# Optimization experiments

Hardware: AMD Instinct MI355X
Metric: run time of the kernel (lower is better)

Reference implementation:

```python
import jax, jax.numpy as jnp
import numpy as np

D = 1024
H = 16
HD = D // H
SCALE = HD ** -0.5
EPS = 1e-5


def _layernorm(x, g, b):
    mu = jnp.mean(x, axis=-1, keepdims=True)
    var = jnp.var(x, axis=-1, keepdims=True)
    return (x - mu) * jax.lax.rsqrt(var + EPS) * g + b


def setup_inputs() -> dict:
    key = jax.random.key(0)
    ks = jax.random.split(key, 10)
    B, L = 2, 2048
    x = jax.random.normal(ks[0], (B, L, D), dtype=jnp.float32)
    s = 1.0 / np.sqrt(D)
    w_qkv = jax.random.normal(ks[1], (D, 3 * D), dtype=jnp.float32) * s
    w_out = jax.random.normal(ks[2], (D, D), dtype=jnp.float32) * s
    w1 = jax.random.normal(ks[3], (D, 2 * D), dtype=jnp.float32) * s
    b1 = jnp.zeros((2 * D,), dtype=jnp.float32)
    w2 = jax.random.normal(ks[4], (2 * D, D), dtype=jnp.float32) / np.sqrt(2 * D)
    b2 = jnp.zeros((D,), dtype=jnp.float32)
    g1 = jnp.ones((D,), dtype=jnp.float32)
    be1 = jnp.zeros((D,), dtype=jnp.float32)
    g2 = jnp.ones((D,), dtype=jnp.float32)
    be2 = jnp.zeros((D,), dtype=jnp.float32)
    return {"x": x, "w_qkv": w_qkv, "w_out": w_out, "w1": w1, "b1": b1,
            "w2": w2, "b2": b2, "g1": g1, "be1": be1, "g2": g2, "be2": be2}


def reference(x, w_qkv, w_out, w1, b1, w2, b2, g1, be1, g2, be2):
    B, L, _ = x.shape
    qkv = (x @ w_qkv).reshape(B, L, 3, H, HD)
    q, k, v = jnp.moveaxis(qkv, 2, 0)          # each [B, L, H, HD]
    # scores: [B, H, L, L]
    attn = jnp.einsum('bqhd,bkhd->bhqk', q, k) * SCALE
    causal = jnp.tril(jnp.ones((L, L), dtype=bool))
    attn = jnp.where(causal[None, None], attn, -jnp.inf)
    attn = jax.nn.softmax(attn, axis=-1)
    out = jnp.einsum('bhqk,bkhd->bqhd', attn, v).reshape(B, L, D)
    out = out @ w_out
    x = _layernorm(x + out, g1, be1)
    ffn = jax.nn.gelu(x @ w1 + b1, approximate=False) @ w2 + b2
    x = _layernorm(x + ffn, g2, be2)
    return x
```

## Files before the change

kernel.cpp:

```cpp
#include <hip/hip_runtime.h>
#include <hip/hip_bf16.h>
#include <math.h>

#define L_SEQ 2048
#define NB 2
#define DM 1024
#define NHEAD 16
#define HDIM 64
#define QKV_LD 3072
#define RL 0.18033688011112042f
#define DTHR 44.3614f

typedef __attribute__((ext_vector_type(8))) __bf16 bf16x8;
typedef __attribute__((ext_vector_type(4))) __bf16 bf16x4;
typedef __attribute__((ext_vector_type(4))) float f32x4;
typedef __attribute__((ext_vector_type(16))) float f32x16;
typedef __attribute__((ext_vector_type(4))) unsigned int u32x4;

typedef __attribute__((address_space(3))) unsigned int lds_u32;
typedef const __attribute__((address_space(1))) unsigned int glob_u32;
#define GLD16(g, l) __builtin_amdgcn_global_load_lds((glob_u32*)(g), (lds_u32*)(l), 16, 0, 0)

__device__ __forceinline__ unsigned pack2(float a, float b) {
  unsigned short ua = __builtin_bit_cast(unsigned short, (__bf16)a);
  unsigned short ub = __builtin_bit_cast(unsigned short, (__bf16)b);
  return (unsigned)ua | ((unsigned)ub << 16);
}

__global__ __launch_bounds__(256) void prep_k(const float* __restrict__ w_qkv,
                                              const float* __restrict__ w_out,
                                              const float* __restrict__ w1,
                                              const float* __restrict__ w2,
                                              const float* __restrict__ x,
                                              __hip_bfloat16* __restrict__ wqT,
                                              __hip_bfloat16* __restrict__ woT,
                                              __hip_bfloat16* __restrict__ w1T,
                                              __hip_bfloat16* __restrict__ w2T,
                                              __hip_bfloat16* __restrict__ xb) {
  const int id = blockIdx.x;
  if (id >= 8192) {
    const size_t base = ((size_t)(id - 8192) * 256 + threadIdx.x) * 8;
    float4 a = *reinterpret_cast<const float4*>(x + base);
    float4 b = *reinterpret_cast<const float4*>(x + base + 4);
    bf16x8 o;
    o[0] = (__bf16)a.x; o[1] = (__bf16)a.y; o[2] = (__bf16)a.z; o[3] = (__bf16)a.w;
    o[4] = (__bf16)b.x; o[5] = (__bf16)b.y; o[6] = (__bf16)b.z; o[7] = (__bf16)b.w;
    *reinterpret_cast<bf16x8*>(xb + base) = o;
    return;
  }
  const float* W; __hip_bfloat16* WT; int K, N, kb, nb;
  if (id < 3072)      { W = w_qkv; WT = wqT; K = 1024; N = 3072; kb = id & 31;          nb = id >> 5; }
  else if (id < 4096) { W = w_out; WT = woT; K = 1024; N = 1024; kb = (id - 3072) & 31; nb = (id - 3072) >> 5; }
  else if (id < 6144) { W = w1;    WT = w1T; K = 1024; N = 2048; kb = (id - 4096) & 31; nb = (id - 4096) >> 5; }
  else                { W = w2;    WT = w2T; K = 2048; N = 1024; kb = (id - 6144) & 63; nb = (id - 6144) >> 6; }
  __shared__ float tsm[32][33];
  const int k0 = kb * 32, n0 = nb * 32;
  const int c = threadIdx.x & 31, r = threadIdx.x >> 5;
#pragma unroll
  for (int i = 0; i < 4; ++i)
    tsm[r + 8 * i][c] = W[(size_t)(k0 + r + 8 * i) * N + n0 + c];
  __syncthreads();
#pragma unroll
  for (int i = 0; i < 4; ++i)
    WT[(size_t)(n0 + r + 8 * i) * K + k0 + c] = __float2bfloat16(tsm[c][r + 8 * i]);
}

template<int EPI, int OUTB, int HASRES, int BN>
__global__ __launch_bounds__(256) void gemm2(const __hip_bfloat16* __restrict__ A,
                                             const __hip_bfloat16* __restrict__ BT,
                                             const float* __restrict__ bias,
                                             float* __restrict__ Cf,
                                             __hip_bfloat16* __restrict__ Cb,
                                             const float* __restrict__ RES,
                                             int M, int N, int K) {
  constexpr int MI = (BN == 128) ? 4 : 2;
  __shared__ __align__(16) __hip_bfloat16 As[128 * 32];
  __shared__ __align__(16) __hip_bfloat16 Bs[BN * 32];
  const int tid  = threadIdx.x;
  const int lane = tid & 63, wave = tid >> 6;
  const int wr = (BN == 128) ? (wave >> 1) : wave;
  const int wc = (BN == 128) ? (wave & 1) : 0;
  const int lr = lane & 15, lq = lane >> 4;
  const int bm0 = blockIdx.y * 128, bn0 = blockIdx.x * BN;
  f32x4 acc[MI][4] = {};

  for (int k0 = 0; k0 < K; k0 += 32) {
#pragma unroll
    for (int j = 0; j < 2; ++j) {
      const int cbase = j * 256 + wave * 64;
      const int c = cbase + lane;
      GLD16(A + (size_t)(bm0 + (c >> 2)) * K + k0 + (c & 3) * 8, (char*)As + cbase * 16);
    }
#pragma unroll
    for (int j = 0; j < BN / 64; ++j) {
      const int cbase = j * 256 + wave * 64;
      const int c = cbase + lane;
      GLD16(BT + (size_t)(bn0 + (c >> 2)) * K + k0 + (c & 3) * 8, (char*)Bs + cbase * 16);
    }
    __syncthreads();
    bf16x8 af[MI], bfr[4];
#pragma unroll
    for (int i = 0; i < MI; ++i)
      af[i] = *reinterpret_cast<const bf16x8*>(As + (wr * (MI * 16) + i * 16 + lr) * 32 + lq * 8);
#pragma unroll
    for (int i = 0; i < 4; ++i)
      bfr[i] = *reinterpret_cast<const bf16x8*>(Bs + (wc * 64 + i * 16 + lr) * 32 + lq * 8);
#pragma unroll
    for (int mi = 0; mi < MI; ++mi)
#pragma unroll
      for (int ni = 0; ni < 4; ++ni)
        acc[mi][ni] = __builtin_amdgcn_mfma_f32_16x16x32_bf16(af[mi], bfr[ni], acc[mi][ni], 0, 0, 0);
    __syncthreads();
  }

#pragma unroll
  for (int mi = 0; mi < MI; ++mi) {
#pragma unroll
    for (int ni = 0; ni < 4; ++ni) {
      const int col = bn0 + wc * 64 + ni * 16 + lr;
      const float bv = (EPI >= 1) ? bias[col] : 0.0f;
#pragma unroll
      for (int j = 0; j < 4; ++j) {
        const int row = bm0 + wr * (MI * 16) + mi * 16 + lq * 4 + j;
        float v = acc[mi][ni][j] + bv;
        if (HASRES) v += RES[(size_t)row * N + col];
        if (EPI == 2) v = 0.5f * v * (1.0f + erff(v * 0.70710678118654752f));
        if (OUTB) Cb[(size_t)row * N + col] = __float2bfloat16(v);
        else      Cf[(size_t)row * N + col] = v;
      }
    }
  }
}


#define DIAG_MASK(sv)                                                               \
  _Pragma("unroll")                                                                 \
  for (int r = 0; r < 16; ++r) {                                                    \
    const int kl = (r & 3) + 8 * (r >> 2) + 4 * hi;                                 \
    if (kl > lq32) sv[r] = -1e30f;                                                  \
  }

#define PV_HALF(wl0, wl1, wh0, wh1, ksg)                                            \
  {                                                                                 \
    unsigned t0_ = hi ? (wl0) : (wh0);                                              \
    unsigned t1_ = hi ? (wl1) : (wh1);                                              \
    t0_ = (unsigned)__shfl_xor((int)t0_, 32);                                       \
    t1_ = (unsigned)__shfl_xor((int)t1_, 32);                                       \
    u32x4 fw;                                                                       \
    fw[0] = hi ? t0_ : (wl0);  fw[1] = hi ? t1_ : (wl1);                            \
    fw[2] = hi ? (wh0) : t0_;  fw[3] = hi ? (wh1) : t1_;                            \
    bf16x8 pfb = __builtin_bit_cast(bf16x8, fw);                                    \
    const int krow_ = (ksg) * 16 + 8 * hi;                                          \
    bf16x8 vA, vB;                                                                  \
    _Pragma("unroll")                                                               \
    for (int j_ = 0; j_ < 8; ++j_) {                                                \
      vA[j_] = VwB[(krow_ + j_) * 64 + lq32];                                       \
      vB[j_] = VwB[(krow_ + j_) * 64 + 32 + lq32];                                  \
    }                                                                               \
    __builtin_amdgcn_s_setprio(1);                                                  \
    o0 = __builtin_amdgcn_mfma_f32_32x32x16_bf16(vA, pfb, o0, 0, 0, 0);             \
    o1 = __builtin_amdgcn_mfma_f32_32x32x16_bf16(vB, pfb, o1, 0, 0, 0);             \
    __builtin_amdgcn_s_setprio(0);                                                  \
  }

__global__ __launch_bounds__(256, 4) void attn_k(const __hip_bfloat16* __restrict__ qkv,
                                                 __hip_bfloat16* __restrict__ outb) {
  __shared__ __align__(16) char smem[4 * 8192 + 2048];
  const int bid = blockIdx.x;
  const int seq = bid >> 3;
  const int bh  = (bid & 7) * 4 + (seq & 3);
  const int qt32 = 63 - (seq >> 2);
  const int b = bh >> 4, h = bh & 15;
  const int qb = qt32 * 32;
  const int tid = threadIdx.x;
  const int lane = tid & 63, wave = tid >> 6;
  const int lq32 = lane & 31, hi = lane >> 5;
  const size_t rowbase = (size_t)(b * L_SEQ) * QKV_LD;
  char* const Vw = smem + wave * 8192;
  const __bf16* const VwB = (const __bf16*)Vw;
  float* const ML = (float*)(smem + 32768);

  bf16x8 qf[4];
  {
    const __hip_bfloat16* qp = qkv + rowbase + (size_t)(qb + lq32) * QKV_LD + h * HDIM + 8 * hi;
#pragma unroll
    for (int c = 0; c < 4; ++c) qf[c] = *reinterpret_cast<const bf16x8*>(qp + 16 * c);
  }

  f32x16 o0 = {}, o1 = {};
  float m = -1e30f, lsum = 0.0f;

  int t = wave;
  bf16x8 kr0, kr1, kr2, kr3;
  if (t <= qt32) {
    const __hip_bfloat16* kp = qkv + rowbase + (size_t)(t * 32 + lq32) * QKV_LD + DM + h * HDIM + 8 * hi;
    kr0 = *reinterpret_cast<const bf16x8*>(kp);
    kr1 = *reinterpret_cast<const bf16x8*>(kp + 16);
    kr2 = *reinterpret_cast<const bf16x8*>(kp + 32);
    kr3 = *reinterpret_cast<const bf16x8*>(kp + 48);
  }

  for (; t <= qt32; t += 4) {
    const int k0 = t * 32;
    const bool pf = (t + 4 <= qt32);
    bf16x8 kn0, kn1, kn2, kn3;
    if (pf) {
      const __hip_bfloat16* kp = qkv + rowbase + (size_t)(k0 + 128 + lq32) * QKV_LD + DM + h * HDIM + 8 * hi;
      kn0 = *reinterpret_cast<const bf16x8*>(kp);
      kn1 = *reinterpret_cast<const bf16x8*>(kp + 16);
      kn2 = *reinterpret_cast<const bf16x8*>(kp + 32);
      kn3 = *reinterpret_cast<const bf16x8*>(kp + 48);
    }
#pragma unroll
    for (int p = 0; p < 4; ++p)
      GLD16(qkv + rowbase + (size_t)(k0 + 8 * p + (lane >> 3)) * QKV_LD + 2 * DM + h * HDIM + (lane & 7) * 8,
            Vw + p * 1024);
    f32x16 s = {};
    __builtin_amdgcn_s_setprio(1);
    s = __builtin_amdgcn_mfma_f32_32x32x16_bf16(kr0, qf[0], s, 0, 0, 0);
    s = __builtin_amdgcn_mfma_f32_32x32x16_bf16(kr1, qf[1], s, 0, 0, 0);
    s = __builtin_amdgcn_mfma_f32_32x32x16_bf16(kr2, qf[2], s, 0, 0, 0);
    s = __builtin_amdgcn_mfma_f32_32x32x16_bf16(kr3, qf[3], s, 0, 0, 0);
    __builtin_amdgcn_s_setprio(0);
    if (t == qt32) { DIAG_MASK(s) }
    float a0 = fmaxf(s[0], s[1]),   a1 = fmaxf(s[2], s[3]);
    float a2 = fmaxf(s[4], s[5]),   a3 = fmaxf(s[6], s[7]);
    float a4 = fmaxf(s[8], s[9]),   a5 = fmaxf(s[10], s[11]);
    float a6 = fmaxf(s[12], s[13]), a7 = fmaxf(s[14], s[15]);
    a0 = fmaxf(a0, a1); a2 = fmaxf(a2, a3); a4 = fmaxf(a4, a5); a6 = fmaxf(a6, a7);
    float tm = fmaxf(fmaxf(a0, a2), fmaxf(a4, a6));
    tm = fmaxf(tm, __shfl_xor(tm, 32));
    if (!__all(tm <= m + DTHR)) {
      const float mn = fmaxf(m, tm);
      const float fac = __builtin_amdgcn_exp2f((m - mn) * RL);
      m = mn; lsum *= fac; o0 *= fac; o1 *= fac;
    }
    const float mneg = -m * RL;
    float rs = 0.0f;
#pragma unroll
    for (int r = 0; r < 16; ++r) {
      s[r] = __builtin_amdgcn_exp2f(fmaf(s[r], RL, mneg));
      rs += s[r];
    }
    rs += __shfl_xor(rs, 32);
    lsum += rs;
    unsigned w0 = pack2(s[0], s[1]),   w1 = pack2(s[2], s[3]);
    unsigned w2 = pack2(s[4], s[5]),   w3 = pack2(s[6], s[7]);
    unsigned w4 = pack2(s[8], s[9]),   w5 = pack2(s[10], s[11]);
    unsigned w6 = pack2(s[12], s[13]), w7 = pack2(s[14], s[15]);
    PV_HALF(w0, w1, w2, w3, 0)
    PV_HALF(w4, w5, w6, w7, 1)
    if (pf) { kr0 = kn0; kr1 = kn1; kr2 = kn2; kr3 = kn3; }
  }

  {
    float* Ow = (float*)Vw;
#pragma unroll
    for (int r = 0; r < 16; ++r) {
      const int d0 = (r & 3) + 8 * (r >> 2) + 4 * hi;
      Ow[d0 * 32 + lq32] = o0[r];
      Ow[(d0 + 32) * 32 + lq32] = o1[r];
    }
    if (hi == 0) {
      ML[wave * 128 + lq32] = m;
      ML[wave * 128 + 64 + lq32] = lsum;
    }
  }
  __syncthreads();

  {
    const int q = tid & 31, dg = tid >> 5;
    const float m0 = ML[q], m1 = ML[128 + q], m2 = ML[256 + q], m3 = ML[384 + q];
    const float M = fmaxf(fmaxf(m0, m1), fmaxf(m2, m3));
    const float c0 = __builtin_amdgcn_exp2f((m0 - M) * RL);
    const float c1 = __builtin_amdgcn_exp2f((m1 - M) * RL);
    const float c2 = __builtin_amdgcn_exp2f((m2 - M) * RL);
    const float c3 = __builtin_amdgcn_exp2f((m3 - M) * RL);
    const float l = c0 * ML[64 + q] + c1 * ML[192 + q] + c2 * ML[320 + q] + c3 * ML[448 + q];
    const float inv = 1.0f / l;
    const float* OB = (const float*)smem;
    bf16x8 ov;
#pragma unroll
    for (int i = 0; i < 8; ++i) {
      const int idx = (dg * 8 + i) * 32 + q;
      const float v = c0 * OB[idx] + c1 * OB[2048 + idx] + c2 * OB[4096 + idx] + c3 * OB[6144 + idx];
      ov[i] = (__bf16)(v * inv);
    }
    *reinterpret_cast<bf16x8*>(outb + (size_t)(b * L_SEQ + qb + q) * DM + h * HDIM + dg * 8) = ov;
  }
}

template<int WB>
__global__ __launch_bounds__(256) void ln_k(const float* __restrict__ X,
                                            const float* __restrict__ g,
                                            const float* __restrict__ be,
                                            float* __restrict__ Y,
                                            __hip_bfloat16* __restrict__ Yb) {
  const int row = blockIdx.x;
  const int tid = threadIdx.x;
  const int lane = tid & 63, wave = tid >> 6;
  float4 x4 = *reinterpret_cast<const float4*>(X + (size_t)row * DM + tid * 4);
  float v0 = x4.x, v1 = x4.y, v2 = x4.z, v3 = x4.w;
  float s  = v0 + v1 + v2 + v3;
  float ss = v0 * v0 + v1 * v1 + v2 * v2 + v3 * v3;
#pragma unroll
  for (int off = 1; off < 64; off <<= 1) {
    s  += __shfl_xor(s, off);
    ss += __shfl_xor(ss, off);
  }
  __shared__ float red[8];
  if (lane == 0) { red[wave] = s; red[4 + wave] = ss; }
  __syncthreads();
  float S  = red[0] + red[1] + red[2] + red[3];
  float SS = red[4] + red[5] + red[6] + red[7];
  float mu  = S * (1.0f / DM);
  float var = SS * (1.0f / DM) - mu * mu;
  float rsd = rsqrtf(var + 1e-5f);
  float4 gv = *reinterpret_cast<const float4*>(g + tid * 4);
  float4 bv = *reinterpret_cast<const float4*>(be + tid * 4);
  float4 y;
  y.x = (v0 - mu) * rsd * gv.x + bv.x;
  y.y = (v1 - mu) * rsd * gv.y + bv.y;
  y.z = (v2 - mu) * rsd * gv.z + bv.z;
  y.w = (v3 - mu) * rsd * gv.w + bv.w;
  *reinterpret_cast<float4*>(Y + (size_t)row * DM + tid * 4) = y;
  if (WB) {
    bf16x4 yb;
    yb[0] = (__bf16)y.x; yb[1] = (__bf16)y.y; yb[2] = (__bf16)y.z; yb[3] = (__bf16)y.w;
    *reinterpret_cast<bf16x4*>(Yb + (size_t)row * DM + tid * 4) = yb;
  }
}

extern "C" void kernel_launch(void* const* d_in, const int* in_sizes, int n_in,
                              void* d_out, int out_size, void* d_ws, size_t ws_size,
                              hipStream_t stream) {
  const float* x     = (const float*)d_in[0];
  const float* w_qkv = (const float*)d_in[1];
  const float* w_out = (const float*)d_in[2];
  const float* w1    = (const float*)d_in[3];
  const float* b1    = (const float*)d_in[4];
  const float* w2    = (const float*)d_in[5];
  const float* b2    = (const float*)d_in[6];
  const float* g1    = (const float*)d_in[7];
  const float* be1   = (const float*)d_in[8];
  const float* g2    = (const float*)d_in[9];
  const float* be2   = (const float*)d_in[10];
  float* outp = (float*)d_out;
  char* base  = (char*)d_ws;
  const int M = NB * L_SEQ;

  __hip_bfloat16* w2T  = (__hip_bfloat16*)(base + 0);
  __hip_bfloat16* woT  = (__hip_bfloat16*)(base + 4194304);
  __hip_bfloat16* w1T  = (__hip_bfloat16*)(base + 6291456);
  __hip_bfloat16* wqT  = (__hip_bfloat16*)(base + 10485760);
  __hip_bfloat16* xb   = (__hip_bfloat16*)(base + 16777216);
  __hip_bfloat16* attnb= xb;
  __hip_bfloat16* qkvb = (__hip_bfloat16*)(base + 25165824);
  __hip_bfloat16* ffh  = (__hip_bfloat16*)(base + 25165824);
  __hip_bfloat16* ln1b = (__hip_bfloat16*)(base + 41943040);
  float*          ffo  = (float*)(base + 8388608);
  float*          ln1f = (float*)(base + 50331648);
  float*          proj = outp;

  prep_k<<<10240, 256, 0, stream>>>(w_qkv, w_out, w1, w2, x, wqT, woT, w1T, w2T, xb);

  gemm2<0, 1, 0, 128><<<dim3(24, 32), 256, 0, stream>>>(xb, wqT, nullptr, nullptr, qkvb, nullptr, M, QKV_LD, DM);
  attn_k<<<2048, 256, 0, stream>>>(qkvb, attnb);
  gemm2<0, 0, 1, 64><<<dim3(16, 32), 256, 0, stream>>>(attnb, woT, nullptr, proj, nullptr, x, M, DM, DM);
  ln_k<1><<<M, 256, 0, stream>>>(proj, g1, be1, ln1f, ln1b);
  gemm2<2, 1, 0, 128><<<dim3(16, 32), 256, 0, stream>>>(ln1b, w1T, b1, nullptr, ffh, nullptr, M, 2 * DM, DM);
  gemm2<1, 0, 1, 64><<<dim3(16, 32), 256, 0, stream>>>(ffh, w2T, b2, ffo, nullptr, ln1f, M, DM, 2 * DM);
  ln_k<0><<<M, 256, 0, stream>>>(ffo, g2, be2, outp, nullptr);
}
```

Before: 221.7 us.

## Transpose V into padded double-buffered LDS and use bf16 LN1 residual

The attention kernel now stages V through registers into a transposed, padded LDS layout, double-buffered one tile ahead. This replaces the per-element strided LDS gathers with vector reads, and K is now loaded at the top of each iteration instead of prefetched. Separately, the first layernorm writes only its bf16 output, and the FFN2 GEMM reads that bf16 tensor as its residual, removing an fp32 write and read. This lowers residual precision and drops the occupancy hint on the attention kernel.

New measurement: 221.6 us. About the same (-0.0%).

```diff
diff --git a/kernel.cpp b/kernel.cpp
--- a/kernel.cpp
+++ b/kernel.cpp
@@ -10,11 +10,16 @@
 #define QKV_LD 3072
 #define RL 0.18033688011112042f
 #define DTHR 44.3614f
+#define VSTRIDE 72
+#define VBUF 4608
+#define WSLICE 9216
+#define WSLICE_F 2304
 
 typedef __attribute__((ext_vector_type(8))) __bf16 bf16x8;
 typedef __attribute__((ext_vector_type(4))) __bf16 bf16x4;
 typedef __attribute__((ext_vector_type(4))) float f32x4;
 typedef __attribute__((ext_vector_type(16))) float f32x16;
+typedef __attribute__((ext_vector_type(8))) unsigned short u16x8;
 typedef __attribute__((ext_vector_type(4))) unsigned int u32x4;
 
 typedef __attribute__((address_space(3))) unsigned int lds_u32;
@@ -71,7 +76,8 @@
                                              const float* __restrict__ bias,
                                              float* __restrict__ Cf,
                                              __hip_bfloat16* __restrict__ Cb,
-                                             const float* __restrict__ RES,
+                                             const float* __restrict__ RESF,
+                                             const __hip_bfloat16* __restrict__ RESB,
                                              int M, int N, int K) {
   constexpr int MI = (BN == 128) ? 4 : 2;
   __shared__ __align__(16) __hip_bfloat16 As[128 * 32];
@@ -123,7 +129,8 @@
       for (int j = 0; j < 4; ++j) {
         const int row = bm0 + wr * (MI * 16) + mi * 16 + lq * 4 + j;
         float v = acc[mi][ni][j] + bv;
-        if (HASRES) v += RES[(size_t)row * N + col];
+        if (HASRES == 1) v += RESF[(size_t)row * N + col];
+        if (HASRES == 2) v += __bfloat162float(RESB[(size_t)row * N + col]);
         if (EPI == 2) v = 0.5f * v * (1.0f + erff(v * 0.70710678118654752f));
         if (OUTB) Cb[(size_t)row * N + col] = __float2bfloat16(v);
         else      Cf[(size_t)row * N + col] = v;
@@ -140,32 +147,55 @@
     if (kl > lq32) sv[r] = -1e30f;                                                  \
   }
 
-#define PV_HALF(wl0, wl1, wh0, wh1, ksg)                                            \
-  {                                                                                 \
-    unsigned t0_ = hi ? (wl0) : (wh0);                                              \
+#define V_STAGE(t_, sel_)                                                           \
+  _Pragma("unroll")                                                                 \
+  for (int c_ = 0; c_ < 2; ++c_) {                                                  \
+    const __hip_bfloat16* vp_ = qkv + rowbase                                       \
+        + (size_t)((t_) * 32 + 4 * kp + 2 * c_) * QKV_LD + 2 * DM + h * HDIM + d8 * 8; \
+    u16x8 lo_ = *reinterpret_cast<const u16x8*>(vp_);                               \
+    u16x8 hi_ = *reinterpret_cast<const u16x8*>(vp_ + QKV_LD);                      \
+    _Pragma("unroll")                                                               \
+    for (int i_ = 0; i_ < 8; ++i_) {                                                \
+      const int d_ = d8 * 8 + i_;                                                   \
+      *reinterpret_cast<unsigned*>(Vw + (sel_) * VBUF + d_ * VSTRIDE                \
+                                   + (4 * kp + 2 * c_) * 2) =                       \
+          (unsigned)lo_[i_] | ((unsigned)hi_[i_] << 16);                            \
+    }                                                                               \
+  }
+
+#define K_LOAD(t_, r0, r1, r2, r3)                                                  \
+  { const __hip_bfloat16* kp_ = qkv + rowbase + (size_t)((t_) * 32 + lq32) * QKV_LD \
+                                + DM + h * HDIM + 8 * hi;                           \
+    r0 = *reinterpret_cast<const bf16x8*>(kp_);                                     \
+    r1 = *reinterpret_cast<const bf16x8*>(kp_ + 16);                                \
+    r2 = *reinterpret_cast<const bf16x8*>(kp_ + 32);                                \
+    r3 = *reinterpret_cast<const bf16x8*>(kp_ + 48); }
+
+#define MK_PF(pf_, wl0, wl1, wh0, wh1)                                              \
+  bf16x8 pf_;                                                                       \
+  { unsigned t0_ = hi ? (wl0) : (wh0);                                              \
     unsigned t1_ = hi ? (wl1) : (wh1);                                              \
     t0_ = (unsigned)__shfl_xor((int)t0_, 32);                                       \
     t1_ = (unsigned)__shfl_xor((int)t1_, 32);                                       \
-    u32x4 fw;                                                                       \
-    fw[0] = hi ? t0_ : (wl0);  fw[1] = hi ? t1_ : (wl1);                            \
-    fw[2] = hi ? (wh0) : t0_;  fw[3] = hi ? (wh1) : t1_;                            \
-    bf16x8 pfb = __builtin_bit_cast(bf16x8, fw);                                    \
-    const int krow_ = (ksg) * 16 + 8 * hi;                                          \
-    bf16x8 vA, vB;                                                                  \
-    _Pragma("unroll")                                                               \
-    for (int j_ = 0; j_ < 8; ++j_) {                                                \
-      vA[j_] = VwB[(krow_ + j_) * 64 + lq32];                                       \
-      vB[j_] = VwB[(krow_ + j_) * 64 + 32 + lq32];                                  \
-    }                                                                               \
-    __builtin_amdgcn_s_setprio(1);                                                  \
-    o0 = __builtin_amdgcn_mfma_f32_32x32x16_bf16(vA, pfb, o0, 0, 0, 0);             \
-    o1 = __builtin_amdgcn_mfma_f32_32x32x16_bf16(vB, pfb, o1, 0, 0, 0);             \
-    __builtin_amdgcn_s_setprio(0);                                                  \
-  }
-
-__global__ __launch_bounds__(256, 4) void attn_k(const __hip_bfloat16* __restrict__ qkv,
-                                                 __hip_bfloat16* __restrict__ outb) {
-  __shared__ __align__(16) char smem[4 * 8192 + 2048];
+    u32x4 fw_;                                                                      \
+    fw_[0] = hi ? t0_ : (wl0);  fw_[1] = hi ? t1_ : (wl1);                          \
+    fw_[2] = hi ? (wh0) : t0_;  fw_[3] = hi ? (wh1) : t1_;                          \
+    pf_ = __builtin_bit_cast(bf16x8, fw_); }
+
+#define PV_READS(ksg_, bb_, vA_, vB_)                                               \
+  bf16x8 vA_, vB_;                                                                  \
+  { const char* pa_ = (bb_) + lq32 * VSTRIDE + 32 * (ksg_) + 16 * hi;               \
+    uint2 a0_ = *reinterpret_cast<const uint2*>(pa_);                               \
+    uint2 a1_ = *reinterpret_cast<const uint2*>(pa_ + 8);                           \
+    const char* pb_ = (bb_) + (32 + lq32) * VSTRIDE + 32 * (ksg_) + 16 * hi;        \
+    uint2 b0_ = *reinterpret_cast<const uint2*>(pb_);                               \
+    uint2 b1_ = *reinterpret_cast<const uint2*>(pb_ + 8);                           \
+    vA_ = __builtin_bit_cast(bf16x8, (u32x4){a0_.x, a0_.y, a1_.x, a1_.y});          \
+    vB_ = __builtin_bit_cast(bf16x8, (u32x4){b0_.x, b0_.y, b1_.x, b1_.y}); }
+
+__global__ __launch_bounds__(256) void attn_k(const __hip_bfloat16* __restrict__ qkv,
+                                              __hip_bfloat16* __restrict__ outb) {
+  __shared__ __align__(16) char smem[4 * WSLICE + 2048];
   const int bid = blockIdx.x;
   const int seq = bid >> 3;
   const int bh  = (bid & 7) * 4 + (seq & 3);
@@ -175,10 +205,10 @@
   const int tid = threadIdx.x;
   const int lane = tid & 63, wave = tid >> 6;
   const int lq32 = lane & 31, hi = lane >> 5;
+  const int kp = lane >> 3, d8 = lane & 7;
   const size_t rowbase = (size_t)(b * L_SEQ) * QKV_LD;
-  char* const Vw = smem + wave * 8192;
-  const __bf16* const VwB = (const __bf16*)Vw;
-  float* const ML = (float*)(smem + 32768);
+  char* const Vw = smem + wave * WSLICE;
+  float* const ML = (float*)(smem + 4 * WSLICE);
 
   bf16x8 qf[4];
   {
@@ -191,30 +221,14 @@
   float m = -1e30f, lsum = 0.0f;
 
   int t = wave;
-  bf16x8 kr0, kr1, kr2, kr3;
-  if (t <= qt32) {
-    const __hip_bfloat16* kp = qkv + rowbase + (size_t)(t * 32 + lq32) * QKV_LD + DM + h * HDIM + 8 * hi;
-    kr0 = *reinterpret_cast<const bf16x8*>(kp);
-    kr1 = *reinterpret_cast<const bf16x8*>(kp + 16);
-    kr2 = *reinterpret_cast<const bf16x8*>(kp + 32);
-    kr3 = *reinterpret_cast<const bf16x8*>(kp + 48);
-  }
+  unsigned sel = 0;
+  if (t <= qt32) { V_STAGE(t, 0) }
 
   for (; t <= qt32; t += 4) {
-    const int k0 = t * 32;
+    bf16x8 kr0, kr1, kr2, kr3;
+    K_LOAD(t, kr0, kr1, kr2, kr3)
     const bool pf = (t + 4 <= qt32);
-    bf16x8 kn0, kn1, kn2, kn3;
-    if (pf) {
-      const __hip_bfloat16* kp = qkv + rowbase + (size_t)(k0 + 128 + lq32) * QKV_LD + DM + h * HDIM + 8 * hi;
-      kn0 = *reinterpret_cast<const bf16x8*>(kp);
-      kn1 = *reinterpret_cast<const bf16x8*>(kp + 16);
-      kn2 = *reinterpret_cast<const bf16x8*>(kp + 32);
-      kn3 = *reinterpret_cast<const bf16x8*>(kp + 48);
-    }
-#pragma unroll
-    for (int p = 0; p < 4; ++p)
-      GLD16(qkv + rowbase + (size_t)(k0 + 8 * p + (lane >> 3)) * QKV_LD + 2 * DM + h * HDIM + (lane & 7) * 8,
-            Vw + p * 1024);
+    if (pf) { V_STAGE(t + 4, sel ^ 1) }
     f32x16 s = {};
     __builtin_amdgcn_s_setprio(1);
     s = __builtin_amdgcn_mfma_f32_32x32x16_bf16(kr0, qf[0], s, 0, 0, 0);
@@ -248,9 +262,18 @@
     unsigned w2 = pack2(s[4], s[5]),   w3 = pack2(s[6], s[7]);
     unsigned w4 = pack2(s[8], s[9]),   w5 = pack2(s[10], s[11]);
     unsigned w6 = pack2(s[12], s[13]), w7 = pack2(s[14], s[15]);
-    PV_HALF(w0, w1, w2, w3, 0)
-    PV_HALF(w4, w5, w6, w7, 1)
-    if (pf) { kr0 = kn0; kr1 = kn1; kr2 = kn2; kr3 = kn3; }
+    MK_PF(pf0, w0, w1, w2, w3)
+    MK_PF(pf1, w4, w5, w6, w7)
+    const char* vb = Vw + sel * VBUF;
+    PV_READS(0, vb, vA0, vB0)
+    PV_READS(1, vb, vA1, vB1)
+    __builtin_amdgcn_s_setprio(1);
+    o0 = __builtin_amdgcn_mfma_f32_32x32x16_bf16(vA0, pf0, o0, 0, 0, 0);
+    o1 = __builtin_amdgcn_mfma_f32_32x32x16_bf16(vB0, pf0, o1, 0, 0, 0);
+    o0 = __builtin_amdgcn_mfma_f32_32x32x16_bf16(vA1, pf1, o0, 0, 0, 0);
+    o1 = __builtin_amdgcn_mfma_f32_32x32x16_bf16(vB1, pf1, o1, 0, 0, 0);
+    __builtin_amdgcn_s_setprio(0);
+    sel ^= 1;
   }
 
   {
@@ -283,14 +306,15 @@
 #pragma unroll
     for (int i = 0; i < 8; ++i) {
       const int idx = (dg * 8 + i) * 32 + q;
-      const float v = c0 * OB[idx] + c1 * OB[2048 + idx] + c2 * OB[4096 + idx] + c3 * OB[6144 + idx];
+      const float v = c0 * OB[idx] + c1 * OB[WSLICE_F + idx]
+                    + c2 * OB[2 * WSLICE_F + idx] + c3 * OB[3 * WSLICE_F + idx];
       ov[i] = (__bf16)(v * inv);
     }
     *reinterpret_cast<bf16x8*>(outb + (size_t)(b * L_SEQ + qb + q) * DM + h * HDIM + dg * 8) = ov;
   }
 }
 
-template<int WB>
+template<int MODE>
 __global__ __launch_bounds__(256) void ln_k(const float* __restrict__ X,
                                             const float* __restrict__ g,
                                             const float* __restrict__ be,
@@ -323,8 +347,9 @@
   y.y = (v1 - mu) * rsd * gv.y + bv.y;
   y.z = (v2 - mu) * rsd * gv.z + bv.z;
   y.w = (v3 - mu) * rsd * gv.w + bv.w;
-  *reinterpret_cast<float4*>(Y + (size_t)row * DM + tid * 4) = y;
-  if (WB) {
+  if (MODE != 2)
+    *reinterpret_cast<float4*>(Y + (size_t)row * DM + tid * 4) = y;
+  if (MODE == 2) {
     bf16x4 yb;
     yb[0] = (__bf16)y.x; yb[1] = (__bf16)y.y; yb[2] = (__bf16)y.z; yb[3] = (__bf16)y.w;
     *reinterpret_cast<bf16x4*>(Yb + (size_t)row * DM + tid * 4) = yb;
@@ -359,16 +384,15 @@
   __hip_bfloat16* ffh  = (__hip_bfloat16*)(base + 25165824);
   __hip_bfloat16* ln1b = (__hip_bfloat16*)(base + 41943040);
   float*          ffo  = (float*)(base + 8388608);
-  float*          ln1f = (float*)(base + 50331648);
   float*          proj = outp;
 
   prep_k<<<10240, 256, 0, stream>>>(w_qkv, w_out, w1, w2, x, wqT, woT, w1T, w2T, xb);
 
-  gemm2<0, 1, 0, 128><<<dim3(24, 32), 256, 0, stream>>>(xb, wqT, nullptr, nullptr, qkvb, nullptr, M, QKV_LD, DM);
+  gemm2<0, 1, 0, 128><<<dim3(24, 32), 256, 0, stream>>>(xb, wqT, nullptr, nullptr, qkvb, nullptr, nullptr, M, QKV_LD, DM);
   attn_k<<<2048, 256, 0, stream>>>(qkvb, attnb);
-  gemm2<0, 0, 1, 64><<<dim3(16, 32), 256, 0, stream>>>(attnb, woT, nullptr, proj, nullptr, x, M, DM, DM);
-  ln_k<1><<<M, 256, 0, stream>>>(proj, g1, be1, ln1f, ln1b);
-  gemm2<2, 1, 0, 128><<<dim3(16, 32), 256, 0, stream>>>(ln1b, w1T, b1, nullptr, ffh, nullptr, M, 2 * DM, DM);
-  gemm2<1, 0, 1, 64><<<dim3(16, 32), 256, 0, stream>>>(ffh, w2T, b2, ffo, nullptr, ln1f, M, DM, 2 * DM);
+  gemm2<0, 0, 1, 64><<<dim3(16, 32), 256, 0, stream>>>(attnb, woT, nullptr, proj, nullptr, x, nullptr, M, DM, DM);
+  ln_k<2><<<M, 256, 0, stream>>>(proj, g1, be1, nullptr, ln1b);
+  gemm2<2, 1, 0, 128><<<dim3(16, 32), 256, 0, stream>>>(ln1b, w1T, b1, nullptr, ffh, nullptr, nullptr, M, 2 * DM, DM);
+  gemm2<1, 0, 2, 64><<<dim3(16, 32), 256, 0, stream>>>(ffh, w2T, b2, ffo, nullptr, nullptr, ln1b, M, DM, 2 * DM);
   ln_k<0><<<M, 256, 0, stream>>>(ffo, g2, be2, outp, nullptr);
 }
```

## Double GEMM K-tile with XOR-swizzled LDS, XCD-aware block remap, bf16 LN1 residual

Applied to the files above, without the earlier changes.

The GEMM now loads 64-wide K tiles per iteration instead of 32. The LDS layout uses an XOR swizzle to avoid bank conflicts on the fragment reads, and this halves the number of barrier pairs per K loop. Blocks are remapped so consecutive block ids are spread across the 8 XCDs, grouping neighbouring tiles on one die for L2 reuse. The first layernorm no longer writes an fp32 copy, and the FFN2 residual reads the bf16 LN1 output instead, which saves memory traffic at the cost of residual precision.

Result: faster. 194.6 us (-12.2%).

```diff
diff --git a/kernel.cpp b/kernel.cpp
--- a/kernel.cpp
+++ b/kernel.cpp
@@ -71,45 +71,60 @@
                                              const float* __restrict__ bias,
                                              float* __restrict__ Cf,
                                              __hip_bfloat16* __restrict__ Cb,
-                                             const float* __restrict__ RES,
+                                             const float* __restrict__ RESF,
+                                             const __hip_bfloat16* __restrict__ RESB,
                                              int M, int N, int K) {
   constexpr int MI = (BN == 128) ? 4 : 2;
-  __shared__ __align__(16) __hip_bfloat16 As[128 * 32];
-  __shared__ __align__(16) __hip_bfloat16 Bs[BN * 32];
+  __shared__ __align__(16) __hip_bfloat16 As[128 * 64];
+  __shared__ __align__(16) __hip_bfloat16 Bs[BN * 64];
   const int tid  = threadIdx.x;
   const int lane = tid & 63, wave = tid >> 6;
   const int wr = (BN == 128) ? (wave >> 1) : wave;
   const int wc = (BN == 128) ? (wave & 1) : 0;
   const int lr = lane & 15, lq = lane >> 4;
-  const int bm0 = blockIdx.y * 128, bn0 = blockIdx.x * BN;
+  unsigned g = blockIdx.y * gridDim.x + blockIdx.x;
+  const unsigned cpx = (gridDim.x * gridDim.y) >> 3;
+  g = (g & 7) * cpx + (g >> 3);
+  const int bm0 = (int)(g / gridDim.x) * 128;
+  const int bn0 = (int)(g % gridDim.x) * BN;
   f32x4 acc[MI][4] = {};
 
-  for (int k0 = 0; k0 < K; k0 += 32) {
-#pragma unroll
-    for (int j = 0; j < 2; ++j) {
+  for (int k0 = 0; k0 < K; k0 += 64) {
+#pragma unroll
+    for (int j = 0; j < 4; ++j) {
       const int cbase = j * 256 + wave * 64;
       const int c = cbase + lane;
-      GLD16(A + (size_t)(bm0 + (c >> 2)) * K + k0 + (c & 3) * 8, (char*)As + cbase * 16);
-    }
-#pragma unroll
-    for (int j = 0; j < BN / 64; ++j) {
+      const int row = c >> 3, slot = c & 7;
+      GLD16(A + (size_t)(bm0 + row) * K + k0 + ((slot ^ (row & 7)) * 8),
+            (char*)As + cbase * 16);
+    }
+#pragma unroll
+    for (int j = 0; j < BN / 32; ++j) {
       const int cbase = j * 256 + wave * 64;
       const int c = cbase + lane;
-      GLD16(BT + (size_t)(bn0 + (c >> 2)) * K + k0 + (c & 3) * 8, (char*)Bs + cbase * 16);
+      const int row = c >> 3, slot = c & 7;
+      GLD16(BT + (size_t)(bn0 + row) * K + k0 + ((slot ^ (row & 7)) * 8),
+            (char*)Bs + cbase * 16);
     }
     __syncthreads();
-    bf16x8 af[MI], bfr[4];
-#pragma unroll
-    for (int i = 0; i < MI; ++i)
-      af[i] = *reinterpret_cast<const bf16x8*>(As + (wr * (MI * 16) + i * 16 + lr) * 32 + lq * 8);
-#pragma unroll
-    for (int i = 0; i < 4; ++i)
-      bfr[i] = *reinterpret_cast<const bf16x8*>(Bs + (wc * 64 + i * 16 + lr) * 32 + lq * 8);
-#pragma unroll
-    for (int mi = 0; mi < MI; ++mi)
-#pragma unroll
-      for (int ni = 0; ni < 4; ++ni)
-        acc[mi][ni] = __builtin_amdgcn_mfma_f32_16x16x32_bf16(af[mi], bfr[ni], acc[mi][ni], 0, 0, 0);
+#pragma unroll
+    for (int kk = 0; kk < 2; ++kk) {
+      const int co = (kk * 64 + lq * 16) ^ ((lr & 7) << 4);
+      bf16x8 af[MI], bfr[4];
+#pragma unroll
+      for (int i = 0; i < MI; ++i)
+        af[i] = *reinterpret_cast<const bf16x8*>(
+            (const char*)As + (wr * (MI * 16) + i * 16 + lr) * 128 + co);
+#pragma unroll
+      for (int i = 0; i < 4; ++i)
+        bfr[i] = *reinterpret_cast<const bf16x8*>(
+            (const char*)Bs + (wc * 64 + i * 16 + lr) * 128 + co);
+#pragma unroll
+      for (int mi = 0; mi < MI; ++mi)
+#pragma unroll
+        for (int ni = 0; ni < 4; ++ni)
+          acc[mi][ni] = __builtin_amdgcn_mfma_f32_16x16x32_bf16(af[mi], bfr[ni], acc[mi][ni], 0, 0, 0);
+    }
     __syncthreads();
   }
 
@@ -123,7 +138,8 @@
       for (int j = 0; j < 4; ++j) {
         const int row = bm0 + wr * (MI * 16) + mi * 16 + lq * 4 + j;
         float v = acc[mi][ni][j] + bv;
-        if (HASRES) v += RES[(size_t)row * N + col];
+        if (HASRES == 1) v += RESF[(size_t)row * N + col];
+        if (HASRES == 2) v += __bfloat162float(RESB[(size_t)row * N + col]);
         if (EPI == 2) v = 0.5f * v * (1.0f + erff(v * 0.70710678118654752f));
         if (OUTB) Cb[(size_t)row * N + col] = __float2bfloat16(v);
         else      Cf[(size_t)row * N + col] = v;
@@ -290,7 +306,7 @@
   }
 }
 
-template<int WB>
+template<int MODE>
 __global__ __launch_bounds__(256) void ln_k(const float* __restrict__ X,
                                             const float* __restrict__ g,
                                             const float* __restrict__ be,
@@ -323,8 +339,9 @@
   y.y = (v1 - mu) * rsd * gv.y + bv.y;
   y.z = (v2 - mu) * rsd * gv.z + bv.z;
   y.w = (v3 - mu) * rsd * gv.w + bv.w;
-  *reinterpret_cast<float4*>(Y + (size_t)row * DM + tid * 4) = y;
-  if (WB) {
+  if (MODE != 2)
+    *reinterpret_cast<float4*>(Y + (size_t)row * DM + tid * 4) = y;
+  if (MODE == 2) {
     bf16x4 yb;
     yb[0] = (__bf16)y.x; yb[1] = (__bf16)y.y; yb[2] = (__bf16)y.z; yb[3] = (__bf16)y.w;
     *reinterpret_cast<bf16x4*>(Yb + (size_t)row * DM + tid * 4) = yb;
@@ -359,16 +376,15 @@
   __hip_bfloat16* ffh  = (__hip_bfloat16*)(base + 25165824);
   __hip_bfloat16* ln1b = (__hip_bfloat16*)(base + 41943040);
   float*          ffo  = (float*)(base + 8388608);
-  float*          ln1f = (float*)(base + 50331648);
   float*          proj = outp;
 
   prep_k<<<10240, 256, 0, stream>>>(w_qkv, w_out, w1, w2, x, wqT, woT, w1T, w2T, xb);
 
-  gemm2<0, 1, 0, 128><<<dim3(24, 32), 256, 0, stream>>>(xb, wqT, nullptr, nullptr, qkvb, nullptr, M, QKV_LD, DM);
+  gemm2<0, 1, 0, 128><<<dim3(24, 32), 256, 0, stream>>>(xb, wqT, nullptr, nullptr, qkvb, nullptr, nullptr, M, QKV_LD, DM);
   attn_k<<<2048, 256, 0, stream>>>(qkvb, attnb);
-  gemm2<0, 0, 1, 64><<<dim3(16, 32), 256, 0, stream>>>(attnb, woT, nullptr, proj, nullptr, x, M, DM, DM);
-  ln_k<1><<<M, 256, 0, stream>>>(proj, g1, be1, ln1f, ln1b);
-  gemm2<2, 1, 0, 128><<<dim3(16, 32), 256, 0, stream>>>(ln1b, w1T, b1, nullptr, ffh, nullptr, M, 2 * DM, DM);
-  gemm2<1, 0, 1, 64><<<dim3(16, 32), 256, 0, stream>>>(ffh, w2T, b2, ffo, nullptr, ln1f, M, DM, 2 * DM);
+  gemm2<0, 0, 1, 64><<<dim3(16, 32), 256, 0, stream>>>(attnb, woT, nullptr, proj, nullptr, x, nullptr, M, DM, DM);
+  ln_k<2><<<M, 256, 0, stream>>>(proj, g1, be1, nullptr, ln1b);
+  gemm2<2, 1, 0, 128><<<dim3(16, 32), 256, 0, stream>>>(ln1b, w1T, b1, nullptr, ffh, nullptr, nullptr, M, 2 * DM, DM);
+  gemm2<1, 0, 2, 64><<<dim3(16, 32), 256, 0, stream>>>(ffh, w2T, b2, ffo, nullptr, nullptr, ln1b, M, DM, 2 * DM);
   ln_k<0><<<M, 256, 0, stream>>>(ffo, g2, be2, outp, nullptr);
 }
```
